# Kernel tuning notes

Measured on AMD Instinct MI355X. Metric: run time of the kernel, lower is better.

## Reference

```python
import jax, jax.numpy as jnp
import numpy as np

DIM = 512
HEADS = 8
DIM_KEY = 32          # dim_key * heads * 2 == DIM (required by the module's own einsum)
NUM_EXPERTS = 65536
NUM_KEYS = 256        # sqrt(NUM_EXPERTS)
TOPK = 16             # product_key_topk == num_experts_per_head
BN_EPS = 1e-5         # flax BatchNorm eps; running stats at init => x / sqrt(1 + eps)


def setup_inputs() -> dict:
    key = jax.random.key(0)
    k1, k2, k3, k4, k5 = jax.random.split(key, 5)
    b, n = 2, 512
    x = jax.random.normal(k1, (b, n, DIM), dtype=jnp.float32)
    # Dense(dim_key*heads*2, use_bias=False): lecun-normal-ish scale
    w_q = jax.random.normal(k2, (DIM, DIM_KEY * HEADS * 2), dtype=jnp.float32) / np.sqrt(DIM)
    # params created with nn.initializers.normal() -> stddev 0.01
    keys = jax.random.normal(k3, (HEADS, NUM_KEYS, 2, DIM_KEY), dtype=jnp.float32) * 0.01
    weight_down_embed = jax.random.normal(k4, (NUM_EXPERTS, DIM), dtype=jnp.float32) * 0.01
    weight_up_embed = jax.random.normal(k5, (NUM_EXPERTS, DIM), dtype=jnp.float32) * 0.01
    return {"x": x, "w_q": w_q, "keys": keys,
            "weight_down_embed": weight_down_embed, "weight_up_embed": weight_up_embed}


def peer_forward(x, w_q, keys, weight_down_embed, weight_up_embed):
    b, n, _ = x.shape
    # to_queries: Dense (no bias) -> BatchNorm in eval mode with init running stats
    # (mean=0, var=1, scale=1, bias=0) -> pure rescale; Dropout(0.0) is identity.
    q = (x @ w_q) * (1.0 / np.sqrt(1.0 + BN_EPS))            # [b, n, DIM]
    # rearrange b n (p h d) -> p b n h d  with p=2
    queries = q.reshape(b, n, 2, HEADS, DIM_KEY).transpose(2, 0, 1, 3, 4)
    sim = jnp.einsum('pbnhd,hkpd->pbnhk', queries, keys)     # [2, b, n, h, NUM_KEYS]
    v0, i0 = jax.lax.top_k(sim[0], TOPK)
    v1, i1 = jax.lax.top_k(sim[1], TOPK)
    # NOTE: faithful to the source's tuple unpacking, which assigns
    # scores_x=v0 (values), scores_y=i0 (indices of axis 0); v1/i1 feed the
    # (unused) all_indices path. So the combined score is values0 + indices0.
    all_scores = v0[..., :, None] + i0[..., None, :].astype(v0.dtype)  # [b,n,h,TOPK,TOPK]
    all_scores = all_scores.reshape(*all_scores.shape[:-2], -1)        # [b,n,h,TOPK*TOPK]
    scores, pk_indices = jax.lax.top_k(all_scores, TOPK)               # [b,n,h,TOPK]
    # Faithful to source: gathers use pk_indices (positions in the TOPK^2 list),
    # NOT the remapped expert ids (`indices` is computed but never used).
    weights_down = jnp.take(weight_down_embed, pk_indices, axis=0)     # [b,n,h,k,DIM]
    weights_up = jnp.take(weight_up_embed, pk_indices, axis=0)         # [b,n,h,k,DIM]
    h = jnp.einsum('bnd,bnhkd->bnhk', q, weights_down)
    h = jax.nn.gelu(h)                                                 # approximate gelu (flax default)
    h = h * jax.nn.softmax(scores, axis=-1)
    out = jnp.einsum('bnhk,bnhkd->bnd', h, weights_up)                 # [b, n, DIM]
    return out


def reference(x, w_q, keys, weight_down_embed, weight_up_embed):
    return peer_forward(x, w_q, keys, weight_down_embed, weight_up_embed)
```

## Files before the change

kernel.cpp:

```cpp
#include <hip/hip_runtime.h>
#include <math.h>

#define DIM    512
#define HEADS  8
#define DK     32
#define NKEYS  256
#define PKTOP  16
#define NTOK   1024

__device__ __forceinline__ float gelu_t(float x)
{
    float x3 = x * x * x;
    return 0.5f * x * (1.f + tanhf(0.7978845608028654f * (x + 0.044715f * x3)));
}

template<int BM, int BN, int BK, int TM, int TN, bool BT, int EPI, bool ZW>
__global__ __launch_bounds__(256)
void sgemm(const float* __restrict__ A, const float* __restrict__ B,
           float* __restrict__ C, int M, int N, int K, float scale,
           float* __restrict__ WS)
{
    __shared__ float As[BK][BM + 4];
    __shared__ float Bs[BK][BN + 4];
    const int tid = threadIdx.x;
    const int tx  = tid & 15;
    const int ty  = tid >> 4;
    const int m0  = blockIdx.y * BM;
    const int n0  = blockIdx.x * BN;

    if (ZW) {
        const int bid = blockIdx.y * gridDim.x + blockIdx.x;
        *(float4*)(WS + (size_t)bid * 1024 + tid * 4) = make_float4(0.f, 0.f, 0.f, 0.f);
    }

    float acc[TM][TN];
#pragma unroll
    for (int i = 0; i < TM; ++i)
#pragma unroll
        for (int j = 0; j < TN; ++j) acc[i][j] = 0.f;

    for (int k0 = 0; k0 < K; k0 += BK) {
#pragma unroll
        for (int it = 0; it < (BM * BK / 4) / 256; ++it) {
            int L   = tid + 256 * it;
            int row = L / (BK / 4), kq = L % (BK / 4);
            float4 v = *(const float4*)(A + (size_t)(m0 + row) * K + k0 + kq * 4);
            As[kq * 4 + 0][row] = v.x; As[kq * 4 + 1][row] = v.y;
            As[kq * 4 + 2][row] = v.z; As[kq * 4 + 3][row] = v.w;
        }
        if (!BT) {
#pragma unroll
            for (int it = 0; it < (BK * BN / 4) / 256; ++it) {
                int L = tid + 256 * it;
                int k = L / (BN / 4), nq = L % (BN / 4);
                float4 v = *(const float4*)(B + (size_t)(k0 + k) * N + n0 + nq * 4);
                *(float4*)&Bs[k][nq * 4] = v;
            }
        } else {
#pragma unroll
            for (int it = 0; it < (BN * BK / 4) / 256; ++it) {
                int L = tid + 256 * it;
                int n = L / (BK / 4), kq = L % (BK / 4);
                float4 v = *(const float4*)(B + (size_t)(n0 + n) * K + k0 + kq * 4);
                Bs[kq * 4 + 0][n] = v.x; Bs[kq * 4 + 1][n] = v.y;
                Bs[kq * 4 + 2][n] = v.z; Bs[kq * 4 + 3][n] = v.w;
            }
        }
        __syncthreads();
#pragma unroll
        for (int k = 0; k < BK; ++k) {
            float a[TM], b[TN];
#pragma unroll
            for (int i = 0; i < TM; ++i) a[i] = As[k][ty * TM + i];
#pragma unroll
            for (int j = 0; j < TN; ++j) b[j] = Bs[k][tx * TN + j];
#pragma unroll
            for (int i = 0; i < TM; ++i)
#pragma unroll
                for (int j = 0; j < TN; ++j) acc[i][j] += a[i] * b[j];
        }
        __syncthreads();
    }
#pragma unroll
    for (int i = 0; i < TM; ++i) {
        int m = m0 + ty * TM + i;
#pragma unroll
        for (int j = 0; j < TN; ++j) {
            int n = n0 + tx * TN + j;
            if (EPI == 1)
                C[(size_t)m * N + n] = gelu_t(acc[i][j]) * WS[(size_t)m * N + n];
            else
                C[(size_t)m * N + n] = acc[i][j] * scale;
        }
    }
}

__device__ __forceinline__ unsigned f2mono(float f)
{
    int b = __float_as_int(f);
    return (unsigned)(b ^ ((b >> 31) | 0x80000000));
}
__device__ __forceinline__ int mbcnt64(unsigned long long m)
{
    return __builtin_amdgcn_mbcnt_hi((unsigned)(m >> 32),
           __builtin_amdgcn_mbcnt_lo((unsigned)m, 0));
}

__device__ __forceinline__ void select_top16(const unsigned u[4], bool sel[4])
{
    unsigned tau = 0;
    for (int bit = 31; bit >= 0; --bit) {
        unsigned t = tau | (1u << bit);
        int cnt = 0;
#pragma unroll
        for (int j = 0; j < 4; ++j)
            cnt += __popcll(__ballot(u[j] >= t));
        if (cnt >= 16) tau = t;
    }
    bool gt[4], eq[4];
    int n_gt = 0, below = 0;
#pragma unroll
    for (int j = 0; j < 4; ++j) {
        gt[j] = (u[j] > tau);
        eq[j] = (u[j] == tau);
        n_gt  += __popcll(__ballot(gt[j]));
        below += mbcnt64(__ballot(eq[j]));
    }
    const int need = 16 - n_gt;
    int run = 0;
#pragma unroll
    for (int j = 0; j < 4; ++j) {
        sel[j] = gt[j] || (eq[j] && (below + run) < need);
        run += eq[j] ? 1 : 0;
    }
}

__global__ __launch_bounds__(256)
void k_simtopk(const float* __restrict__ q, const float* __restrict__ keys,
               float* __restrict__ wsum)
{
    __shared__ float Sv[4][16];
    __shared__ int   Sc[4][16];
    __shared__ float V0[4][16];
    __shared__ int   I0[4][16];

    const int wid  = threadIdx.x >> 6;
    const int lane = threadIdx.x & 63;
    const int th   = blockIdx.x * 4 + wid;
    const int t    = th >> 3;
    const int hh   = th & 7;
    const int base = lane * 4;

    const float4* qv = (const float4*)(q + (size_t)t * DIM + hh * DK);
    float4 qr[8];
#pragma unroll
    for (int i = 0; i < 8; ++i) qr[i] = qv[i];

    float v1[4];
#pragma unroll
    for (int j = 0; j < 4; ++j) {
        const float4* kv = (const float4*)(keys + ((size_t)hh * NKEYS + base + j) * 2 * DK);
        float s = 0.f;
#pragma unroll
        for (int i = 0; i < 8; ++i) {
            float4 kk = kv[i];
            s += kk.x * qr[i].x + kk.y * qr[i].y + kk.z * qr[i].z + kk.w * qr[i].w;
        }
        v1[j] = s;
    }

    unsigned u1[4];
#pragma unroll
    for (int j = 0; j < 4; ++j) u1[j] = f2mono(v1[j]);
    bool sel1[4];
    select_top16(u1, sel1);

    int below = 0;
#pragma unroll
    for (int j = 0; j < 4; ++j) below += mbcnt64(__ballot(sel1[j]));
    int run = 0;
#pragma unroll
    for (int j = 0; j < 4; ++j) {
        if (sel1[j]) { Sv[wid][below + run] = v1[j]; Sc[wid][below + run] = base + j; }
        run += sel1[j] ? 1 : 0;
    }
    __syncthreads();

    {
        float mv = Sv[wid][lane & 15];
        int   mc = Sc[wid][lane & 15];
        int rank = 0;
#pragma unroll
        for (int k = 0; k < 16; ++k) {
            float ov = Sv[wid][k];
            int   oc = Sc[wid][k];
            rank += (ov > mv || (ov == mv && oc < mc)) ? 1 : 0;
        }
        if (lane < 16) { V0[wid][rank] = mv; I0[wid][rank] = mc; }
    }
    __syncthreads();

    const float v0v = V0[wid][lane >> 2];
    const int4  iv  = *(const int4*)&I0[wid][(lane & 3) * 4];
    float f[4];
    f[0] = v0v + (float)iv.x; f[1] = v0v + (float)iv.y;
    f[2] = v0v + (float)iv.z; f[3] = v0v + (float)iv.w;
    unsigned u2[4];
#pragma unroll
    for (int j = 0; j < 4; ++j) u2[j] = f2mono(f[j]);
    bool sel2[4];
    select_top16(u2, sel2);

    int mi = max(max(iv.x, iv.y), max(iv.z, iv.w));
    mi = max(mi, __shfl_xor(mi, 1, 64));
    mi = max(mi, __shfl_xor(mi, 2, 64));
    const float mx = V0[wid][0] + (float)mi;

    float e[4];
    float s = 0.f;
#pragma unroll
    for (int j = 0; j < 4; ++j) {
        e[j] = sel2[j] ? expf(f[j] - mx) : 0.f;
        s += e[j];
    }
#pragma unroll
    for (int off = 32; off; off >>= 1) s += __shfl_xor(s, off, 64);
    const float inv = 1.f / s;

#pragma unroll
    for (int j = 0; j < 4; ++j)
        if (sel2[j])
            atomicAdd(&wsum[(size_t)t * NKEYS + base + j], e[j] * inv);
}

extern "C" void kernel_launch(void* const* d_in, const int* in_sizes, int n_in,
                              void* d_out, int out_size, void* d_ws, size_t ws_size,
                              hipStream_t stream)
{
    const float* x    = (const float*)d_in[0];
    const float* wq   = (const float*)d_in[1];
    const float* keys = (const float*)d_in[2];
    const float* wd   = (const float*)d_in[3];
    const float* wu   = (const float*)d_in[4];
    float* out = (float*)d_out;

    float* q    = (float*)d_ws;
    float* Cb   = q + NTOK * DIM;
    float* wsum = Cb + NTOK * NKEYS;

    const float bnscale = 1.0f / sqrtf(1.0f + 1e-5f);

    sgemm<32, 64, 64, 2, 4, false, 0, true>
        <<<dim3(DIM / 64, NTOK / 32), 256, 0, stream>>>(x, wq, q, NTOK, DIM, DIM,
                                                        bnscale, wsum);

    k_simtopk<<<dim3(NTOK * HEADS / 4), 256, 0, stream>>>(q, keys, wsum);

    sgemm<32, 32, 64, 2, 2, true, 1, false>
        <<<dim3(NKEYS / 32, NTOK / 32), 256, 0, stream>>>(q, wd, Cb, NTOK, NKEYS,
                                                          DIM, 1.f, wsum);

    sgemm<32, 64, 64, 2, 4, false, 0, false>
        <<<dim3(DIM / 64, NTOK / 32), 256, 0, stream>>>(Cb, wu, out, NTOK, DIM,
                                                        NKEYS, 1.f, wsum);
}
```

Before: 322.4 us.

## Stage per-head keys in swizzled LDS and process several tokens per block

New measurement: 289.5 us, median of 2. 1.11x faster.

```diff
diff --git a/kernel.cpp b/kernel.cpp
--- a/kernel.cpp
+++ b/kernel.cpp
@@ -106,131 +106,171 @@
            __builtin_amdgcn_mbcnt_lo((unsigned)m, 0));
 }
 
-__device__ __forceinline__ void select_top16(const unsigned u[4], bool sel[4])
-{
-    unsigned tau = 0;
+__device__ __forceinline__ void find_tau(const unsigned u[4],
+                                         unsigned &tau_o, int &need_o)
+{
+    unsigned tau = 0u;
     for (int bit = 31; bit >= 0; --bit) {
         unsigned t = tau | (1u << bit);
         int cnt = 0;
 #pragma unroll
         for (int j = 0; j < 4; ++j)
             cnt += __popcll(__ballot(u[j] >= t));
-        if (cnt >= 16) tau = t;
-    }
-    bool gt[4], eq[4];
-    int n_gt = 0, below = 0;
-#pragma unroll
-    for (int j = 0; j < 4; ++j) {
-        gt[j] = (u[j] > tau);
-        eq[j] = (u[j] == tau);
-        n_gt  += __popcll(__ballot(gt[j]));
-        below += mbcnt64(__ballot(eq[j]));
-    }
-    const int need = 16 - n_gt;
-    int run = 0;
-#pragma unroll
-    for (int j = 0; j < 4; ++j) {
-        sel[j] = gt[j] || (eq[j] && (below + run) < need);
-        run += eq[j] ? 1 : 0;
-    }
+        if (cnt >= 16) {
+            tau = t;
+            if (cnt == 16) break;
+        }
+    }
+    int n_gt = 0;
+#pragma unroll
+    for (int j = 0; j < 4; ++j)
+        n_gt += __popcll(__ballot(u[j] > tau));
+    need_o = 16 - n_gt;
+    tau_o  = tau;
 }
 
 __global__ __launch_bounds__(256)
 void k_simtopk(const float* __restrict__ q, const float* __restrict__ keys,
                float* __restrict__ wsum)
 {
+    __shared__ float Ks[NKEYS][32];
     __shared__ float Sv[4][16];
     __shared__ int   Sc[4][16];
     __shared__ float V0[4][16];
     __shared__ int   I0[4][16];
 
-    const int wid  = threadIdx.x >> 6;
-    const int lane = threadIdx.x & 63;
-    const int th   = blockIdx.x * 4 + wid;
-    const int t    = th >> 3;
-    const int hh   = th & 7;
-    const int base = lane * 4;
-
-    const float4* qv = (const float4*)(q + (size_t)t * DIM + hh * DK);
-    float4 qr[8];
-#pragma unroll
-    for (int i = 0; i < 8; ++i) qr[i] = qv[i];
-
-    float v1[4];
-#pragma unroll
-    for (int j = 0; j < 4; ++j) {
-        const float4* kv = (const float4*)(keys + ((size_t)hh * NKEYS + base + j) * 2 * DK);
+    const int hh   = blockIdx.x & 7;
+    const int tg   = blockIdx.x >> 3;
+    const int tid  = threadIdx.x;
+    const int wid  = tid >> 6;
+    const int lane = tid & 63;
+
+#pragma unroll
+    for (int it = 0; it < 8; ++it) {
+        int idx = it * 1024 + tid * 4;
+        int r = idx >> 5, d = idx & 31;
+        float4 v = *(const float4*)(keys + ((size_t)hh * NKEYS + r) * 2 * DK + d);
+        *(float4*)&Ks[r][d ^ ((r & 7) * 4)] = v;
+    }
+    __syncthreads();
+
+    const int sw = (lane & 7) * 4;
+
+    for (int ti = 0; ti < 4; ++ti) {
+        const int t = tg * 16 + wid * 4 + ti;
+
+        const float4* qv = (const float4*)(q + (size_t)t * DIM + hh * DK);
+        float4 qr[8];
+#pragma unroll
+        for (int i = 0; i < 8; ++i) qr[i] = qv[i];
+
+        float v1[4];
+#pragma unroll
+        for (int j = 0; j < 4; ++j) {
+            const float* kr = &Ks[lane + 64 * j][0];
+            float s = 0.f;
+#pragma unroll
+            for (int d0 = 0; d0 < 8; ++d0) {
+                float4 kk = *(const float4*)&kr[(d0 * 4) ^ sw];
+                s += kk.x * qr[d0].x + kk.y * qr[d0].y
+                   + kk.z * qr[d0].z + kk.w * qr[d0].w;
+            }
+            v1[j] = s;
+        }
+
+        unsigned u1[4];
+#pragma unroll
+        for (int j = 0; j < 4; ++j) u1[j] = f2mono(v1[j]);
+        unsigned tau1; int need1;
+        find_tau(u1, tau1, need1);
+
+        bool sel1[4];
+        {
+            int pre = 0;
+#pragma unroll
+            for (int j = 0; j < 4; ++j) {
+                bool gt = u1[j] > tau1, eq = u1[j] == tau1;
+                unsigned long long bal = __ballot(eq);
+                sel1[j] = gt || (eq && (pre + mbcnt64(bal)) < need1);
+                pre += __popcll(bal);
+            }
+        }
+        {
+            int pre = 0;
+#pragma unroll
+            for (int j = 0; j < 4; ++j) {
+                unsigned long long bal = __ballot(sel1[j]);
+                int pos = pre + mbcnt64(bal);
+                if (sel1[j]) { Sv[wid][pos] = v1[j]; Sc[wid][pos] = lane + 64 * j; }
+                pre += __popcll(bal);
+            }
+        }
+        __syncthreads();
+
+        {
+            float mv = Sv[wid][lane & 15];
+            int   mc = Sc[wid][lane & 15];
+            int rank = 0;
+#pragma unroll
+            for (int k = 0; k < 16; ++k) {
+                float ov = Sv[wid][k];
+                int   oc = Sc[wid][k];
+                rank += (ov > mv || (ov == mv && oc < mc)) ? 1 : 0;
+            }
+            if (lane < 16) { V0[wid][rank] = mv; I0[wid][rank] = mc; }
+        }
+        __syncthreads();
+
+        const float v0v = V0[wid][lane >> 2];
+        const int4  iv  = *(const int4*)&I0[wid][(lane & 3) * 4];
+        float f[4];
+        f[0] = v0v + (float)iv.x; f[1] = v0v + (float)iv.y;
+        f[2] = v0v + (float)iv.z; f[3] = v0v + (float)iv.w;
+        unsigned u2[4];
+#pragma unroll
+        for (int j = 0; j < 4; ++j) u2[j] = f2mono(f[j]);
+        unsigned tau2; int need2;
+        find_tau(u2, tau2, need2);
+
+        bool sel2[4];
+        {
+            bool gt2[4], eq2[4];
+            int below = 0;
+#pragma unroll
+            for (int j = 0; j < 4; ++j) {
+                gt2[j] = u2[j] > tau2;
+                eq2[j] = u2[j] == tau2;
+                below += mbcnt64(__ballot(eq2[j]));
+            }
+            int run = 0;
+#pragma unroll
+            for (int j = 0; j < 4; ++j) {
+                sel2[j] = gt2[j] || (eq2[j] && (below + run) < need2);
+                run += eq2[j] ? 1 : 0;
+            }
+        }
+
+        int mi = max(max(iv.x, iv.y), max(iv.z, iv.w));
+        mi = max(mi, __shfl_xor(mi, 1, 64));
+        mi = max(mi, __shfl_xor(mi, 2, 64));
+        const float mx = V0[wid][0] + (float)mi;
+
+        float e[4];
         float s = 0.f;
 #pragma unroll
-        for (int i = 0; i < 8; ++i) {
-            float4 kk = kv[i];
-            s += kk.x * qr[i].x + kk.y * qr[i].y + kk.z * qr[i].z + kk.w * qr[i].w;
-        }
-        v1[j] = s;
-    }
-
-    unsigned u1[4];
-#pragma unroll
-    for (int j = 0; j < 4; ++j) u1[j] = f2mono(v1[j]);
-    bool sel1[4];
-    select_top16(u1, sel1);
-
-    int below = 0;
-#pragma unroll
-    for (int j = 0; j < 4; ++j) below += mbcnt64(__ballot(sel1[j]));
-    int run = 0;
-#pragma unroll
-    for (int j = 0; j < 4; ++j) {
-        if (sel1[j]) { Sv[wid][below + run] = v1[j]; Sc[wid][below + run] = base + j; }
-        run += sel1[j] ? 1 : 0;
-    }
-    __syncthreads();
-
-    {
-        float mv = Sv[wid][lane & 15];
-        int   mc = Sc[wid][lane & 15];
-        int rank = 0;
-#pragma unroll
-        for (int k = 0; k < 16; ++k) {
-            float ov = Sv[wid][k];
-            int   oc = Sc[wid][k];
-            rank += (ov > mv || (ov == mv && oc < mc)) ? 1 : 0;
-        }
-        if (lane < 16) { V0[wid][rank] = mv; I0[wid][rank] = mc; }
-    }
-    __syncthreads();
-
-    const float v0v = V0[wid][lane >> 2];
-    const int4  iv  = *(const int4*)&I0[wid][(lane & 3) * 4];
-    float f[4];
-    f[0] = v0v + (float)iv.x; f[1] = v0v + (float)iv.y;
-    f[2] = v0v + (float)iv.z; f[3] = v0v + (float)iv.w;
-    unsigned u2[4];
-#pragma unroll
-    for (int j = 0; j < 4; ++j) u2[j] = f2mono(f[j]);
-    bool sel2[4];
-    select_top16(u2, sel2);
-
-    int mi = max(max(iv.x, iv.y), max(iv.z, iv.w));
-    mi = max(mi, __shfl_xor(mi, 1, 64));
-    mi = max(mi, __shfl_xor(mi, 2, 64));
-    const float mx = V0[wid][0] + (float)mi;
-
-    float e[4];
-    float s = 0.f;
-#pragma unroll
-    for (int j = 0; j < 4; ++j) {
-        e[j] = sel2[j] ? expf(f[j] - mx) : 0.f;
-        s += e[j];
-    }
-#pragma unroll
-    for (int off = 32; off; off >>= 1) s += __shfl_xor(s, off, 64);
-    const float inv = 1.f / s;
-
-#pragma unroll
-    for (int j = 0; j < 4; ++j)
-        if (sel2[j])
-            atomicAdd(&wsum[(size_t)t * NKEYS + base + j], e[j] * inv);
+        for (int j = 0; j < 4; ++j) {
+            e[j] = sel2[j] ? expf(f[j] - mx) : 0.f;
+            s += e[j];
+        }
+#pragma unroll
+        for (int off = 32; off; off >>= 1) s += __shfl_xor(s, off, 64);
+        const float inv = 1.f / s;
+
+#pragma unroll
+        for (int j = 0; j < 4; ++j)
+            if (sel2[j])
+                atomicAdd(&wsum[(size_t)t * NKEYS + lane * 4 + j], e[j] * inv);
+    }
 }
 
 extern "C" void kernel_launch(void* const* d_in, const int* in_sizes, int n_in,
@@ -254,7 +294,7 @@
         <<<dim3(DIM / 64, NTOK / 32), 256, 0, stream>>>(x, wq, q, NTOK, DIM, DIM,
                                                         bnscale, wsum);
 
-    k_simtopk<<<dim3(NTOK * HEADS / 4), 256, 0, stream>>>(q, keys, wsum);
+    k_simtopk<<<dim3(HEADS * 64), 256, 0, stream>>>(q, keys, wsum);
 
     sgemm<32, 32, 64, 2, 2, true, 1, false>
         <<<dim3(NKEYS / 32, NTOK / 32), 256, 0, stream>>>(q, wd, Cb, NTOK, NKEYS,
```
